# Kernel optimization log

Measured on AMD Instinct MI355X. Metric: run time of the kernel, lower is better.

## Reference

```python
import jax, jax.numpy as jnp
import numpy as np

V, E, H, F, A, L = 32000, 256, 512, 512, 256, 49  # vocab, embed, hidden, feature, attn, n_locations
B, T = 64, 32


def setup_inputs() -> dict:
    key = jax.random.key(0)
    ks = jax.random.split(key, 16)
    s = lambda k, sh: (jax.random.normal(k, sh, jnp.float32) * 0.02)
    embedding = s(ks[0], (V, E)).at[0].set(0.0)  # padding_idx=0 row zeroed
    return dict(
        image_feats=jax.random.normal(ks[1], (B, L, F), jnp.float32),
        caption_in=jax.random.randint(ks[2], (B, T), 0, V, dtype=jnp.int32),
        embedding=embedding,
        W_init_h=s(ks[3], (F, H)), b_init_h=jnp.zeros((H,), jnp.float32),
        W_init_c=s(ks[4], (F, H)), b_init_c=jnp.zeros((H,), jnp.float32),
        W_feat=s(ks[5], (F, A)), b_feat=jnp.zeros((A,), jnp.float32),
        W_hid=s(ks[6], (H, A)), b_hid=jnp.zeros((A,), jnp.float32),
        W_score=s(ks[7], (A,)), b_score=jnp.zeros((), jnp.float32),
        W_ih=s(ks[8], (E + F, 4 * H)), b_ih=jnp.zeros((4 * H,), jnp.float32),
        W_hh=s(ks[9], (H, 4 * H)), b_hh=jnp.zeros((4 * H,), jnp.float32),
        W_out=s(ks[10], (H, V)), b_out=jnp.zeros((V,), jnp.float32),
    )


def reference(image_feats, caption_in, embedding,
              W_init_h, b_init_h, W_init_c, b_init_c,
              W_feat, b_feat, W_hid, b_hid, W_score, b_score,
              W_ih, b_ih, W_hh, b_hh, W_out, b_out):
    # init_hidden_state: mean over spatial locations -> two linears
    mean_feats = image_feats.mean(axis=1)                      # (B, F)
    h0 = mean_feats @ W_init_h + b_init_h                      # (B, H)
    c0 = mean_feats @ W_init_c + b_init_c                      # (B, H)
    embs = embedding[caption_in]                               # (B, T, E); dropout = identity (eval)
    feat_proj = image_feats @ W_feat + b_feat                  # (B, L, A) - invariant over t, precompute

    def step(carry, emb_t):
        h, c = carry
        # additive attention
        energy = jnp.tanh(feat_proj + (h @ W_hid + b_hid)[:, None, :])   # (B, L, A)
        scores = energy @ W_score + b_score                              # (B, L)
        alpha = jax.nn.softmax(scores, axis=1)                           # (B, L)
        context = jnp.einsum('bl,blf->bf', alpha, image_feats)           # (B, F)
        # LSTMCell (torch gate order i, f, g, o)
        x = jnp.concatenate([emb_t, context], axis=1)                    # (B, E+F)
        gates = x @ W_ih + b_ih + h @ W_hh + b_hh                        # (B, 4H)
        i, f, g, o = jnp.split(gates, 4, axis=1)
        i = jax.nn.sigmoid(i); f = jax.nn.sigmoid(f); o = jax.nn.sigmoid(o)
        c_new = f * c + i * jnp.tanh(g)
        h_new = o * jnp.tanh(c_new)
        logits_t = h_new @ W_out + b_out                                 # (B, V); dropout = identity
        return (h_new, c_new), (logits_t, alpha)

    _, (logits, alphas) = jax.lax.scan(step, (h0, c0), jnp.swapaxes(embs, 0, 1))
    predictions = jnp.swapaxes(logits, 0, 1)   # (B, T, V)
    all_alphas = jnp.swapaxes(alphas, 0, 1)    # (B, T, L)
    return predictions, all_alphas
```

## Files before the change

### kernel.cpp

```cpp
#include <hip/hip_runtime.h>
#include <hip/hip_bf16.h>

typedef _Float16 f16;
typedef _Float16 f16x8 __attribute__((ext_vector_type(8)));
typedef _Float16 f16x4 __attribute__((ext_vector_type(4)));
typedef _Float16 f16x2 __attribute__((ext_vector_type(2)));
typedef float f32x4 __attribute__((ext_vector_type(4)));
typedef unsigned long long ull;

#define B_ 64
#define T_ 32
#define L_ 49
#define F_ 512
#define H_ 512
#define A_ 256
#define E_ 256
#define V_ 32000
#define G4 2048
#define NG 64
#define NLOG 125
#define SLOT 16

#define ALOAD32(p)     __hip_atomic_load((const unsigned*)(p), __ATOMIC_RELAXED, __HIP_MEMORY_SCOPE_AGENT)
#define ASTORE32(p, v) __hip_atomic_store((unsigned*)(p), (v), __ATOMIC_RELAXED, __HIP_MEMORY_SCOPE_AGENT)
#define ASTORE64(p, v) __hip_atomic_store((ull*)(p), (v), __ATOMIC_RELAXED, __HIP_MEMORY_SCOPE_AGENT)

#if defined(__has_builtin)
#if __has_builtin(__builtin_amdgcn_fdot2)
#define HAS_FDOT2 1
#endif
#endif

#define NB_EMBG 256
#define NB_Q    128
#define NB_INIT 64
#define NB_FP   196

struct Smem128 { f16 As[128][40]; f16 Bs[128][40]; };

__global__ __launch_bounds__(256) void k_prep(
    const float* __restrict__ image_feats, const int* __restrict__ caption,
    const float* __restrict__ embedding,
    const float* __restrict__ W_init_h, const float* __restrict__ b_init_h,
    const float* __restrict__ W_init_c, const float* __restrict__ b_init_c,
    const float* __restrict__ W_feat, const float* __restrict__ b_feat,
    const float* __restrict__ W_hid, const float* __restrict__ W_ih,
    const float* __restrict__ b_ih, const float* __restrict__ b_hh,
    f16* __restrict__ embP, f16* __restrict__ Whidp,
    f16* __restrict__ hslab, float* __restrict__ c_cur,
    float* __restrict__ featproj) {
    __shared__ __align__(16) char smem[32768];
    int bid = blockIdx.x, tid = threadIdx.x;
    int r = bid;
    if (r < NB_EMBG) {
        Smem128* sm = (Smem128*)smem;
        int mtiles = B_ * T_ / 128;
        int m0 = (r % mtiles) * 128, n0 = (r / mtiles) * 128;
        int lane = tid & 63, wave = tid >> 6;
        int wr = (wave >> 1) * 64, wc = (wave & 1) * 64;
        int frow = lane & 15, fk = (lane >> 4) * 8;
        int ra = tid >> 2, ka = (tid & 3) * 8;
        int kb = tid >> 3, nb = (tid & 7) * 16;
        int tok0 = caption[m0 + ra], tok1 = caption[m0 + 64 + ra];
        f32x4 acc[4][4];
#pragma unroll
        for (int i = 0; i < 4; ++i)
#pragma unroll
            for (int j = 0; j < 4; ++j) { acc[i][j][0]=0.f; acc[i][j][1]=0.f; acc[i][j][2]=0.f; acc[i][j][3]=0.f; }
        for (int k0 = 0; k0 < E_; k0 += 32) {
            float4 e00 = *(const float4*)&embedding[(size_t)tok0 * E_ + k0 + ka];
            float4 e01 = *(const float4*)&embedding[(size_t)tok0 * E_ + k0 + ka + 4];
            float4 e10 = *(const float4*)&embedding[(size_t)tok1 * E_ + k0 + ka];
            float4 e11 = *(const float4*)&embedding[(size_t)tok1 * E_ + k0 + ka + 4];
            const float* wrow = W_ih + (size_t)(k0 + kb) * G4 + n0 + nb;
            float4 w0 = *(const float4*)wrow;
            float4 w1 = *(const float4*)(wrow + 4);
            float4 w2 = *(const float4*)(wrow + 8);
            float4 w3 = *(const float4*)(wrow + 12);
            __syncthreads();
            {
                f16x8 a0 = {(f16)e00.x,(f16)e00.y,(f16)e00.z,(f16)e00.w,
                            (f16)e01.x,(f16)e01.y,(f16)e01.z,(f16)e01.w};
                f16x8 a1 = {(f16)e10.x,(f16)e10.y,(f16)e10.z,(f16)e10.w,
                            (f16)e11.x,(f16)e11.y,(f16)e11.z,(f16)e11.w};
                *(f16x8*)&sm->As[ra][ka] = a0;
                *(f16x8*)&sm->As[64 + ra][ka] = a1;
                float wv[16] = {w0.x,w0.y,w0.z,w0.w, w1.x,w1.y,w1.z,w1.w,
                                w2.x,w2.y,w2.z,w2.w, w3.x,w3.y,w3.z,w3.w};
#pragma unroll
                for (int j = 0; j < 16; ++j) sm->Bs[nb + j][kb] = (f16)wv[j];
            }
            __syncthreads();
            f16x8 av[4], bv[4];
#pragma unroll
            for (int i = 0; i < 4; ++i) {
                av[i] = *(f16x8*)&sm->As[wr + i * 16 + frow][fk];
                bv[i] = *(f16x8*)&sm->Bs[wc + i * 16 + frow][fk];
            }
#pragma unroll
            for (int mi = 0; mi < 4; ++mi)
#pragma unroll
                for (int ni = 0; ni < 4; ++ni)
                    acc[mi][ni] = __builtin_amdgcn_mfma_f32_16x16x32_f16(av[mi], bv[ni], acc[mi][ni], 0, 0, 0);
        }
        int rq = (lane >> 4) * 4;
#pragma unroll
        for (int mi = 0; mi < 4; ++mi)
#pragma unroll
            for (int ni = 0; ni < 4; ++ni) {
                int cc = n0 + wc + ni * 16 + frow;
                float badd = b_ih[cc] + b_hh[cc];
#pragma unroll
                for (int rr2 = 0; rr2 < 4; ++rr2) {
                    int rr = m0 + wr + mi * 16 + rq + rr2;
                    embP[((size_t)rr * 512 + (cc & 511)) * 4 + (cc >> 9)] =
                        (f16)(acc[mi][ni][rr2] + badd);
                }
            }
        return;
    }
    r -= NB_EMBG;
    if (r < NB_Q) {
        int k4 = r;
        f16 buf[4];
#pragma unroll
        for (int j = 0; j < 4; ++j) buf[j] = (f16)W_hid[(size_t)(4 * k4 + j) * 256 + tid];
        *(f16x4*)&Whidp[((size_t)k4 * 256 + tid) * 4] = *(f16x4*)buf;
        return;
    }
    r -= NB_Q;
    if (r < NB_INIT) {
        float* mean = (float*)smem;
        int b = r;
        for (int f = tid; f < F_; f += 256) {
            float s = 0.f;
            for (int l = 0; l < L_; ++l) s += image_feats[((size_t)b * L_ + l) * F_ + f];
            mean[f] = s * (1.f / 49.f);
        }
        __syncthreads();
        for (int h = tid; h < H_; h += 256) {
            float a = b_init_h[h], c = b_init_c[h];
            for (int k = 0; k < F_; ++k) {
                float m = mean[k];
                a += m * W_init_h[k * H_ + h];
                c += m * W_init_c[k * H_ + h];
            }
            hslab[(size_t)b * H_ + h] = (f16)a;
            c_cur[b * H_ + h] = c;
        }
        return;
    }
    r -= NB_INIT;
    {
        float (*fs)[F_] = (float(*)[F_])smem;
        int r0 = r * 16;
        for (int i = tid; i < 16 * F_; i += 256)
            fs[i >> 9][i & 511] = image_feats[(size_t)r0 * F_ + i];
        __syncthreads();
        float acc[16];
#pragma unroll
        for (int q = 0; q < 16; ++q) acc[q] = 0.f;
        for (int k = 0; k < F_; ++k) {
            float w = W_feat[k * A_ + tid];
#pragma unroll
            for (int q = 0; q < 16; ++q) acc[q] += fs[q][k] * w;
        }
        float bb = b_feat[tid];
#pragma unroll
        for (int q = 0; q < 16; ++q) featproj[(size_t)(r0 + q) * A_ + tid] = acc[q] + bb;
    }
}

struct GateSm {
    float fp[L_][A_];
    unsigned fe[L_ * 256];
    float ea[A_];
    float ws[A_];
    float sc[64];
    float alpha[64];
    unsigned hL[256];
};
struct GemmSm {
    f16 w[32][512];
    f16 w2[32][512];
    union {
        f16 hs[64][512];
        f16 hwT16[64][40];
    } u;
};
struct LogSm { f16 hs[128][512]; };

__device__ __forceinline__ void wait_n(const unsigned* flags, int n, unsigned target) {
    int tid = threadIdx.x;
    if (tid < n) {
        const unsigned* p = flags + tid * SLOT;
        while (ALOAD32(p) < target) __builtin_amdgcn_s_sleep(1);
    }
    asm volatile("" ::: "memory");
    __syncthreads();
}
__device__ __forceinline__ void wait_n_slow(const unsigned* flags, int n, unsigned target) {
    int tid = threadIdx.x;
    if (tid < n) {
        const unsigned* p = flags + tid * SLOT;
        while (ALOAD32(p) < target) __builtin_amdgcn_s_sleep(8);
    }
    asm volatile("" ::: "memory");
    __syncthreads();
}

__device__ __forceinline__ float sigm(float x) { return 1.f / (1.f + __expf(-x)); }
__device__ __forceinline__ float tanh_f(float x) { return 1.f - 2.f / (1.f + __expf(2.f * x)); }

__global__ __launch_bounds__(256, 1) void k_steps(
    const float* __restrict__ W_hh, const float* __restrict__ W_ih,
    const f16* __restrict__ Whidp,
    const float* __restrict__ featproj, const float* __restrict__ image_feats,
    const float* __restrict__ b_hid,
    const float* __restrict__ W_score, const float* __restrict__ b_score,
    const f16* __restrict__ embP, const float* __restrict__ c_cur,
    f16* __restrict__ hslab, f16* __restrict__ ctxslab, f16* __restrict__ hwcslab,
    const float* __restrict__ W_out, f16* __restrict__ WoutT,
    const float* __restrict__ b_out,
    float* __restrict__ preds, float* __restrict__ out_alpha,
    unsigned* __restrict__ gateflag, unsigned* __restrict__ ctxflag,
    unsigned* __restrict__ gemmflag) {
    __shared__ __align__(16) char smraw[sizeof(LogSm)];
    int bid = blockIdx.x, tid = threadIdx.x;

    if (bid < 64) {
        int b = bid;
        GateSm* S = (GateSm*)smraw;
        for (int i = tid; i < L_ * A_; i += 256)
            ((float*)S->fp)[i] = featproj[(size_t)b * L_ * A_ + i];
        {
            const float2* src = (const float2*)(image_feats + (size_t)b * L_ * F_);
            for (int i = tid; i < L_ * 256; i += 256) {
                float2 v = src[i];
                union { f16 h[2]; unsigned u; } pk;
                pk.h[0] = (f16)v.x; pk.h[1] = (f16)v.y;
                S->fe[i] = pk.u;
            }
        }
        S->ws[tid] = W_score[tid];
        float bhid_r = b_hid[tid];
        float bsc = b_score[0];
        S->hL[tid] = ((const unsigned*)hslab)[(size_t)b * 256 + tid];
        float cs0 = c_cur[b * H_ + 2 * tid], cs1 = c_cur[b * H_ + 2 * tid + 1];
        const f16x4* wp4 = (const f16x4*)Whidp;
        int wv = tid >> 6, ln = tid & 63;
        __syncthreads();

        for (int t = 0; t < T_; ++t) {
            {
                float acc = bhid_r;
#pragma unroll 16
                for (int k4 = 0; k4 < 128; ++k4) {
                    union { f16x4 v; f16x2 p[2]; } w;
                    w.v = wp4[(size_t)k4 * 256 + tid];
                    union { unsigned u; f16x2 v; } h0, h1;
                    h0.u = S->hL[2 * k4];
                    h1.u = S->hL[2 * k4 + 1];
#ifdef HAS_FDOT2
                    acc = __builtin_amdgcn_fdot2(w.p[0], h0.v, acc, false);
                    acc = __builtin_amdgcn_fdot2(w.p[1], h1.v, acc, false);
#else
                    acc += (float)w.p[0].x * (float)h0.v.x + (float)w.p[0].y * (float)h0.v.y;
                    acc += (float)w.p[1].x * (float)h1.v.x + (float)w.p[1].y * (float)h1.v.y;
#endif
                }
                S->ea[tid] = acc;
            }
            __syncthreads();
            for (int l = wv; l < L_; l += 4) {
                float p = 0.f;
#pragma unroll
                for (int q = 0; q < 4; ++q) {
                    int j = ln + q * 64;
                    p += tanh_f(S->fp[l][j] + S->ea[j]) * S->ws[j];
                }
#pragma unroll
                for (int off = 32; off > 0; off >>= 1) p += __shfl_xor(p, off);
                if (ln == 0) S->sc[l] = p;
            }
            __syncthreads();
            if (tid < 64) {
                float v = (tid < L_) ? S->sc[tid] + bsc : -3.4e38f;
                float m = v;
#pragma unroll
                for (int off = 32; off > 0; off >>= 1) m = fmaxf(m, __shfl_xor(m, off));
                float e = (tid < L_) ? __expf(v - m) : 0.f;
                float s = e;
#pragma unroll
                for (int off = 32; off > 0; off >>= 1) s += __shfl_xor(s, off);
                if (tid < L_) {
                    float al = e / s;
                    S->alpha[tid] = al;
                    out_alpha[((size_t)b * T_ + t) * L_ + tid] = al;
                }
            }
            __syncthreads();
            {
                float c0 = 0.f, c1 = 0.f;
#pragma unroll 7
                for (int l = 0; l < L_; ++l) {
                    float a = S->alpha[l];
                    union { unsigned u; f16x2 v; } fv;
                    fv.u = S->fe[l * 256 + tid];
                    c0 += a * (float)fv.v.x;
                    c1 += a * (float)fv.v.y;
                }
                union { f16 h[2]; unsigned u; } pk;
                pk.h[0] = (f16)c0; pk.h[1] = (f16)c1;
                ASTORE32((unsigned*)ctxslab + ((size_t)t * B_ + b) * 256 + tid, pk.u);
            }
            __syncthreads();
            if (tid == 0) ASTORE32(&ctxflag[b * SLOT], (unsigned)(t + 1));
            f16x8 ep = *(const f16x8*)&embP[((size_t)b * T_ + t) * G4 + 8 * tid];
            wait_n(gemmflag, NG, (unsigned)(t + 1));
            {
                f16x8 hw = *(const f16x8*)&hwcslab[((size_t)t * B_ + b) * G4 + 8 * tid];
                float gA[8];
#pragma unroll
                for (int i = 0; i < 8; ++i) gA[i] = (float)hw[i] + (float)ep[i];
                float cn0 = sigm(gA[1]) * cs0 + sigm(gA[0]) * tanh_f(gA[2]);
                float cn1 = sigm(gA[5]) * cs1 + sigm(gA[4]) * tanh_f(gA[6]);
                float hn0 = sigm(gA[3]) * tanh_f(cn0);
                float hn1 = sigm(gA[7]) * tanh_f(cn1);
                cs0 = cn0; cs1 = cn1;
                union { f16 h[2]; unsigned u; } pk;
                pk.h[0] = (f16)hn0; pk.h[1] = (f16)hn1;
                S->hL[tid] = pk.u;
                ASTORE32((unsigned*)hslab + ((size_t)(t + 1) * B_ + b) * 256 + tid, pk.u);
            }
            __syncthreads();
            if (tid == 0)
                ASTORE32(&gateflag[b * SLOT], (unsigned)(t + 2));
        }
    } else if (bid < 64 + NG) {
        int g = bid - 64;
        GemmSm* S = (GemmSm*)smraw;
        for (int rowbase = 0; rowbase < 512; rowbase += 256) {
            int k = rowbase + tid;
            const float* wh = W_hh + (size_t)k * G4 + 8 * g;
            const float* wi = W_ih + (size_t)(E_ + k) * G4 + 8 * g;
            int ch = k >> 3, j = k & 7;
#pragma unroll
            for (int q = 0; q < 4; ++q) {
                float4 v0 = *(const float4*)(wh + q * 512);
                float4 v1 = *(const float4*)(wh + q * 512 + 4);
                float4 u0 = *(const float4*)(wi + q * 512);
                float4 u1 = *(const float4*)(wi + q * 512 + 4);
                float vv[8] = {v0.x,v0.y,v0.z,v0.w, v1.x,v1.y,v1.z,v1.w};
                float uu[8] = {u0.x,u0.y,u0.z,u0.w, u1.x,u1.y,u1.z,u1.w};
#pragma unroll
                for (int d = 0; d < 8; ++d) {
                    int r = d * 4 + q;
                    S->w[r][((ch ^ (r & 7)) << 3) + j]  = (f16)vv[d];
                    S->w2[r][((ch ^ (r & 7)) << 3) + j] = (f16)uu[d];
                }
            }
        }
        int wvv = tid >> 6, lane = tid & 63;
        int frow = lane & 15, q = lane >> 4, sw = frow & 7, rq = q * 4;
        int mb = (wvv >> 1) * 32, c16 = (wvv & 1) * 16;
        int bo = tid >> 2, cq = (tid & 3) * 8;
        __syncthreads();

        for (int t = 0; t < T_; ++t) {
            if (t) wait_n(gateflag, 64, (unsigned)(t + 1));
            {
                const f16* hsrc = hslab + (size_t)t * B_ * H_;
#pragma unroll
                for (int i = 0; i < 16; ++i) {
                    int idx = i * 256 + tid;
                    int r = idx >> 6, ch = idx & 63;
                    *(f16x8*)&S->u.hs[r][(ch ^ (r & 7)) * 8] =
                        *(const f16x8*)&hsrc[(size_t)r * H_ + ch * 8];
                }
            }
            __syncthreads();
            f32x4 a4[2];
            a4[0][0]=0.f; a4[0][1]=0.f; a4[0][2]=0.f; a4[0][3]=0.f;
            a4[1][0]=0.f; a4[1][1]=0.f; a4[1][2]=0.f; a4[1][3]=0.f;
#pragma unroll
            for (int kk = 0; kk < 16; ++kk) {
                int ch = ((kk * 4 + q) ^ sw) * 8;
                f16x8 bv = *(f16x8*)&S->w[c16 + frow][ch];
                f16x8 av0 = *(f16x8*)&S->u.hs[mb + frow][ch];
                f16x8 av1 = *(f16x8*)&S->u.hs[mb + 16 + frow][ch];
                a4[0] = __builtin_amdgcn_mfma_f32_16x16x32_f16(av0, bv, a4[0], 0, 0, 0);
                a4[1] = __builtin_amdgcn_mfma_f32_16x16x32_f16(av1, bv, a4[1], 0, 0, 0);
            }
            wait_n(ctxflag, 64, (unsigned)(t + 1));
            {
                const f16* csrc = ctxslab + (size_t)t * B_ * F_;
#pragma unroll
                for (int i = 0; i < 16; ++i) {
                    int idx = i * 256 + tid;
                    int r = idx >> 6, ch = idx & 63;
                    *(f16x8*)&S->u.hs[r][(ch ^ (r & 7)) * 8] =
                        *(const f16x8*)&csrc[(size_t)r * F_ + ch * 8];
                }
            }
            __syncthreads();
#pragma unroll
            for (int kk = 0; kk < 16; ++kk) {
                int ch = ((kk * 4 + q) ^ sw) * 8;
                f16x8 bv = *(f16x8*)&S->w2[c16 + frow][ch];
                f16x8 av0 = *(f16x8*)&S->u.hs[mb + frow][ch];
                f16x8 av1 = *(f16x8*)&S->u.hs[mb + 16 + frow][ch];
                a4[0] = __builtin_amdgcn_mfma_f32_16x16x32_f16(av0, bv, a4[0], 0, 0, 0);
                a4[1] = __builtin_amdgcn_mfma_f32_16x16x32_f16(av1, bv, a4[1], 0, 0, 0);
            }
            __syncthreads();
#pragma unroll
            for (int mi = 0; mi < 2; ++mi)
#pragma unroll
                for (int r = 0; r < 4; ++r)
                    S->u.hwT16[mb + mi * 16 + rq + r][c16 + frow] = (f16)a4[mi][r];
            __syncthreads();
            {
                f16* dst = hwcslab + ((size_t)t * B_ + bo) * G4 + 32 * g + cq;
                union { f16 h[4]; ull u; } pk0, pk1;
                *(f16x4*)pk0.h = *(f16x4*)&S->u.hwT16[bo][cq];
                *(f16x4*)pk1.h = *(f16x4*)&S->u.hwT16[bo][cq + 4];
                ASTORE64(dst, pk0.u);
                ASTORE64(dst + 4, pk1.u);
            }
            __syncthreads();
            if (tid == 0)
                ASTORE32(&gemmflag[g * SLOT], (unsigned)(t + 1));
        }
    } else {
        int nt = bid - 64 - NG;
        int n0 = nt * 256;
        LogSm* S = (LogSm*)smraw;
        int wvv = tid >> 6, lane = tid & 63;
        int frow = lane & 15, q = lane >> 4, sw = frow & 7, rq = q * 4;

        {
            float (*ls)[33] = (float(*)[33])smraw;
            int rr = tid >> 3, cs = (tid & 7) * 4;
            int cr = tid >> 3, rs = (tid & 7) * 4;
            for (int c0 = 0; c0 < 256; c0 += 32)
                for (int k0 = 0; k0 < 512; k0 += 32) {
                    float4 v = *(const float4*)&W_out[(size_t)(k0 + rr) * V_ + n0 + c0 + cs];
                    __syncthreads();
                    ls[rr][cs] = v.x; ls[rr][cs + 1] = v.y; ls[rr][cs + 2] = v.z; ls[rr][cs + 3] = v.w;
                    __syncthreads();
                    f16x4 o = {(f16)ls[rs][cr], (f16)ls[rs + 1][cr],
                               (f16)ls[rs + 2][cr], (f16)ls[rs + 3][cr]};
                    *(f16x4*)&WoutT[(size_t)(n0 + c0 + cr) * 512 + k0 + rs] = o;
                }
            __syncthreads();
        }

        for (int tc = 0; tc < T_ / 2; ++tc) {
            wait_n_slow(gateflag, 64, (unsigned)(2 * tc + 3));
            {
                const f16* hsrc = hslab + (size_t)(2 * tc + 1) * B_ * H_;
#pragma unroll
                for (int i = 0; i < 32; ++i) {
                    int idx = i * 256 + tid;
                    int r = idx >> 6, ch = idx & 63;
                    *(f16x8*)&S->hs[r][(ch ^ (r & 7)) * 8] =
                        *(const f16x8*)&hsrc[(size_t)r * H_ + ch * 8];
                }
            }
            __syncthreads();
            f32x4 acc[8][4];
#pragma unroll
            for (int mi = 0; mi < 8; ++mi)
#pragma unroll
                for (int ni = 0; ni < 4; ++ni) { acc[mi][ni][0]=0.f; acc[mi][ni][1]=0.f; acc[mi][ni][2]=0.f; acc[mi][ni][3]=0.f; }
#pragma unroll 2
            for (int kk = 0; kk < 16; ++kk) {
                int ch = ((kk * 4 + q) ^ sw) * 8;
                f16x8 av[8], bv[4];
#pragma unroll
                for (int mi = 0; mi < 8; ++mi)
                    av[mi] = *(f16x8*)&S->hs[mi * 16 + frow][ch];
#pragma unroll
                for (int ni = 0; ni < 4; ++ni)
                    bv[ni] = *(const f16x8*)&WoutT[(size_t)(n0 + wvv * 64 + ni * 16 + frow) * 512 + kk * 32 + q * 8];
#pragma unroll
                for (int mi = 0; mi < 8; ++mi)
#pragma unroll
                    for (int ni = 0; ni < 4; ++ni)
                        acc[mi][ni] = __builtin_amdgcn_mfma_f32_16x16x32_f16(av[mi], bv[ni], acc[mi][ni], 0, 0, 0);
            }
#pragma unroll
            for (int ni = 0; ni < 4; ++ni) {
                int cc = n0 + wvv * 64 + ni * 16 + frow;
                float badd = b_out[cc];
#pragma unroll
                for (int mi = 0; mi < 8; ++mi)
#pragma unroll
                    for (int r = 0; r < 4; ++r) {
                        int rr = mi * 16 + rq + r;
                        int tt = 2 * tc + (rr >> 6), bb2 = rr & 63;
                        preds[((size_t)bb2 * T_ + tt) * V_ + cc] = acc[mi][ni][r] + badd;
                    }
            }
            __syncthreads();
        }
    }
}

extern "C" void kernel_launch(void* const* d_in, const int* in_sizes, int n_in,
                              void* d_out, int out_size, void* d_ws, size_t ws_size,
                              hipStream_t stream) {
    const float* image_feats = (const float*)d_in[0];
    const int*   caption     = (const int*)d_in[1];
    const float* embedding   = (const float*)d_in[2];
    const float* W_init_h    = (const float*)d_in[3];
    const float* b_init_h    = (const float*)d_in[4];
    const float* W_init_c    = (const float*)d_in[5];
    const float* b_init_c    = (const float*)d_in[6];
    const float* W_feat      = (const float*)d_in[7];
    const float* b_feat      = (const float*)d_in[8];
    const float* W_hid       = (const float*)d_in[9];
    const float* b_hid       = (const float*)d_in[10];
    const float* W_score     = (const float*)d_in[11];
    const float* b_score     = (const float*)d_in[12];
    const float* W_ih        = (const float*)d_in[13];
    const float* b_ih        = (const float*)d_in[14];
    const float* W_hh        = (const float*)d_in[15];
    const float* b_hh        = (const float*)d_in[16];
    const float* W_out       = (const float*)d_in[17];
    const float* b_out       = (const float*)d_in[18];

    float* preds = (float*)d_out;
    float* out_alpha = preds + (size_t)B_ * T_ * V_;

    size_t off = 0;
    char* base = (char*)d_ws;
    auto carve = [&](size_t bytes) {
        void* p = base + off;
        off += (bytes + 255) & ~(size_t)255;
        return p;
    };
    f16* embP       = (f16*)carve((size_t)B_ * T_ * G4 * 2);
    float* featproj = (float*)carve((size_t)B_ * L_ * A_ * 4);
    float* c_cur    = (float*)carve((size_t)B_ * H_ * 4);
    f16* hslab      = (f16*)carve((size_t)(T_ + 1) * B_ * H_ * 2);
    f16* ctxslab    = (f16*)carve((size_t)T_ * B_ * F_ * 2);
    f16* hwcslab    = (f16*)carve((size_t)T_ * B_ * G4 * 2);
    unsigned* flags = (unsigned*)carve((64 + 64 + NG) * SLOT * 4);
    f16* WoutT      = (f16*)carve((size_t)V_ * H_ * 2);
    f16* Whidp      = (f16*)carve((size_t)H_ * A_ * 2);
    unsigned* gateflag = flags;
    unsigned* ctxflag  = flags + 64 * SLOT;
    unsigned* gemmflag = flags + 128 * SLOT;
    (void)ws_size; (void)in_sizes; (void)n_in; (void)out_size;

    hipMemsetAsync(flags, 0, (64 + 64 + NG) * SLOT * 4, stream);
    hipLaunchKernelGGL(k_prep, dim3(NB_EMBG + NB_Q + NB_INIT + NB_FP), dim3(256), 0, stream,
                       image_feats, caption, embedding,
                       W_init_h, b_init_h, W_init_c, b_init_c,
                       W_feat, b_feat, W_hid, W_ih, b_ih, b_hh,
                       embP, Whidp, hslab, c_cur, featproj);
    hipLaunchKernelGGL(k_steps, dim3(64 + NG + NLOG), dim3(256), 0, stream,
                       W_hh, W_ih, Whidp, featproj, image_feats, b_hid,
                       W_score, b_score, embP, c_cur,
                       hslab, ctxslab, hwcslab,
                       W_out, WoutT, b_out, preds, out_alpha,
                       gateflag, ctxflag, gemmflag);
}
```

Before: 624.3 us.

## Move init, feat-proj and W_hid packing into persistent kernel; split recurrent GEMM

```diff
diff --git a/kernel.cpp b/kernel.cpp
--- a/kernel.cpp
+++ b/kernel.cpp
@@ -31,149 +31,84 @@
 #endif
 #endif
 
-#define NB_EMBG 256
-#define NB_Q    128
-#define NB_INIT 64
-#define NB_FP   196
-
 struct Smem128 { f16 As[128][40]; f16 Bs[128][40]; };
 
 __global__ __launch_bounds__(256) void k_prep(
-    const float* __restrict__ image_feats, const int* __restrict__ caption,
-    const float* __restrict__ embedding,
-    const float* __restrict__ W_init_h, const float* __restrict__ b_init_h,
-    const float* __restrict__ W_init_c, const float* __restrict__ b_init_c,
-    const float* __restrict__ W_feat, const float* __restrict__ b_feat,
-    const float* __restrict__ W_hid, const float* __restrict__ W_ih,
+    const int* __restrict__ caption, const float* __restrict__ embedding,
+    const float* __restrict__ W_ih,
     const float* __restrict__ b_ih, const float* __restrict__ b_hh,
-    f16* __restrict__ embP, f16* __restrict__ Whidp,
-    f16* __restrict__ hslab, float* __restrict__ c_cur,
-    float* __restrict__ featproj) {
-    __shared__ __align__(16) char smem[32768];
-    int bid = blockIdx.x, tid = threadIdx.x;
-    int r = bid;
-    if (r < NB_EMBG) {
-        Smem128* sm = (Smem128*)smem;
-        int mtiles = B_ * T_ / 128;
-        int m0 = (r % mtiles) * 128, n0 = (r / mtiles) * 128;
-        int lane = tid & 63, wave = tid >> 6;
-        int wr = (wave >> 1) * 64, wc = (wave & 1) * 64;
-        int frow = lane & 15, fk = (lane >> 4) * 8;
-        int ra = tid >> 2, ka = (tid & 3) * 8;
-        int kb = tid >> 3, nb = (tid & 7) * 16;
-        int tok0 = caption[m0 + ra], tok1 = caption[m0 + 64 + ra];
-        f32x4 acc[4][4];
-#pragma unroll
-        for (int i = 0; i < 4; ++i)
-#pragma unroll
-            for (int j = 0; j < 4; ++j) { acc[i][j][0]=0.f; acc[i][j][1]=0.f; acc[i][j][2]=0.f; acc[i][j][3]=0.f; }
-        for (int k0 = 0; k0 < E_; k0 += 32) {
-            float4 e00 = *(const float4*)&embedding[(size_t)tok0 * E_ + k0 + ka];
-            float4 e01 = *(const float4*)&embedding[(size_t)tok0 * E_ + k0 + ka + 4];
-            float4 e10 = *(const float4*)&embedding[(size_t)tok1 * E_ + k0 + ka];
-            float4 e11 = *(const float4*)&embedding[(size_t)tok1 * E_ + k0 + ka + 4];
-            const float* wrow = W_ih + (size_t)(k0 + kb) * G4 + n0 + nb;
-            float4 w0 = *(const float4*)wrow;
-            float4 w1 = *(const float4*)(wrow + 4);
-            float4 w2 = *(const float4*)(wrow + 8);
-            float4 w3 = *(const float4*)(wrow + 12);
-            __syncthreads();
-            {
-                f16x8 a0 = {(f16)e00.x,(f16)e00.y,(f16)e00.z,(f16)e00.w,
-                            (f16)e01.x,(f16)e01.y,(f16)e01.z,(f16)e01.w};
-                f16x8 a1 = {(f16)e10.x,(f16)e10.y,(f16)e10.z,(f16)e10.w,
-                            (f16)e11.x,(f16)e11.y,(f16)e11.z,(f16)e11.w};
-                *(f16x8*)&sm->As[ra][ka] = a0;
-                *(f16x8*)&sm->As[64 + ra][ka] = a1;
-                float wv[16] = {w0.x,w0.y,w0.z,w0.w, w1.x,w1.y,w1.z,w1.w,
-                                w2.x,w2.y,w2.z,w2.w, w3.x,w3.y,w3.z,w3.w};
-#pragma unroll
-                for (int j = 0; j < 16; ++j) sm->Bs[nb + j][kb] = (f16)wv[j];
-            }
-            __syncthreads();
-            f16x8 av[4], bv[4];
-#pragma unroll
-            for (int i = 0; i < 4; ++i) {
-                av[i] = *(f16x8*)&sm->As[wr + i * 16 + frow][fk];
-                bv[i] = *(f16x8*)&sm->Bs[wc + i * 16 + frow][fk];
-            }
-#pragma unroll
-            for (int mi = 0; mi < 4; ++mi)
-#pragma unroll
-                for (int ni = 0; ni < 4; ++ni)
-                    acc[mi][ni] = __builtin_amdgcn_mfma_f32_16x16x32_f16(av[mi], bv[ni], acc[mi][ni], 0, 0, 0);
-        }
-        int rq = (lane >> 4) * 4;
+    f16* __restrict__ embP) {
+    __shared__ Smem128 sm;
+    int tid = threadIdx.x;
+    int mtiles = B_ * T_ / 128;
+    int m0 = ((int)blockIdx.x % mtiles) * 128, n0 = ((int)blockIdx.x / mtiles) * 128;
+    int lane = tid & 63, wave = tid >> 6;
+    int wr = (wave >> 1) * 64, wc = (wave & 1) * 64;
+    int frow = lane & 15, fk = (lane >> 4) * 8;
+    int ra = tid >> 2, ka = (tid & 3) * 8;
+    int kb = tid >> 3, nb = (tid & 7) * 16;
+    int tok0 = caption[m0 + ra], tok1 = caption[m0 + 64 + ra];
+    f32x4 acc[4][4];
+#pragma unroll
+    for (int i = 0; i < 4; ++i)
+#pragma unroll
+        for (int j = 0; j < 4; ++j) { acc[i][j][0]=0.f; acc[i][j][1]=0.f; acc[i][j][2]=0.f; acc[i][j][3]=0.f; }
+    for (int k0 = 0; k0 < E_; k0 += 32) {
+        float4 e00 = *(const float4*)&embedding[(size_t)tok0 * E_ + k0 + ka];
+        float4 e01 = *(const float4*)&embedding[(size_t)tok0 * E_ + k0 + ka + 4];
+        float4 e10 = *(const float4*)&embedding[(size_t)tok1 * E_ + k0 + ka];
+        float4 e11 = *(const float4*)&embedding[(size_t)tok1 * E_ + k0 + ka + 4];
+        const float* wrow = W_ih + (size_t)(k0 + kb) * G4 + n0 + nb;
+        float4 w0 = *(const float4*)wrow;
+        float4 w1 = *(const float4*)(wrow + 4);
+        float4 w2 = *(const float4*)(wrow + 8);
+        float4 w3 = *(const float4*)(wrow + 12);
+        __syncthreads();
+        {
+            f16x8 a0 = {(f16)e00.x,(f16)e00.y,(f16)e00.z,(f16)e00.w,
+                        (f16)e01.x,(f16)e01.y,(f16)e01.z,(f16)e01.w};
+            f16x8 a1 = {(f16)e10.x,(f16)e10.y,(f16)e10.z,(f16)e10.w,
+                        (f16)e11.x,(f16)e11.y,(f16)e11.z,(f16)e11.w};
+            *(f16x8*)&sm.As[ra][ka] = a0;
+            *(f16x8*)&sm.As[64 + ra][ka] = a1;
+            float wv[16] = {w0.x,w0.y,w0.z,w0.w, w1.x,w1.y,w1.z,w1.w,
+                            w2.x,w2.y,w2.z,w2.w, w3.x,w3.y,w3.z,w3.w};
+#pragma unroll
+            for (int j = 0; j < 16; ++j) sm.Bs[nb + j][kb] = (f16)wv[j];
+        }
+        __syncthreads();
+        f16x8 av[4], bv[4];
+#pragma unroll
+        for (int i = 0; i < 4; ++i) {
+            av[i] = *(f16x8*)&sm.As[wr + i * 16 + frow][fk];
+            bv[i] = *(f16x8*)&sm.Bs[wc + i * 16 + frow][fk];
+        }
 #pragma unroll
         for (int mi = 0; mi < 4; ++mi)
 #pragma unroll
-            for (int ni = 0; ni < 4; ++ni) {
-                int cc = n0 + wc + ni * 16 + frow;
-                float badd = b_ih[cc] + b_hh[cc];
-#pragma unroll
-                for (int rr2 = 0; rr2 < 4; ++rr2) {
-                    int rr = m0 + wr + mi * 16 + rq + rr2;
-                    embP[((size_t)rr * 512 + (cc & 511)) * 4 + (cc >> 9)] =
-                        (f16)(acc[mi][ni][rr2] + badd);
-                }
-            }
-        return;
+            for (int ni = 0; ni < 4; ++ni)
+                acc[mi][ni] = __builtin_amdgcn_mfma_f32_16x16x32_f16(av[mi], bv[ni], acc[mi][ni], 0, 0, 0);
     }
-    r -= NB_EMBG;
-    if (r < NB_Q) {
-        int k4 = r;
-        f16 buf[4];
-#pragma unroll
-        for (int j = 0; j < 4; ++j) buf[j] = (f16)W_hid[(size_t)(4 * k4 + j) * 256 + tid];
-        *(f16x4*)&Whidp[((size_t)k4 * 256 + tid) * 4] = *(f16x4*)buf;
-        return;
-    }
-    r -= NB_Q;
-    if (r < NB_INIT) {
-        float* mean = (float*)smem;
-        int b = r;
-        for (int f = tid; f < F_; f += 256) {
-            float s = 0.f;
-            for (int l = 0; l < L_; ++l) s += image_feats[((size_t)b * L_ + l) * F_ + f];
-            mean[f] = s * (1.f / 49.f);
-        }
-        __syncthreads();
-        for (int h = tid; h < H_; h += 256) {
-            float a = b_init_h[h], c = b_init_c[h];
-            for (int k = 0; k < F_; ++k) {
-                float m = mean[k];
-                a += m * W_init_h[k * H_ + h];
-                c += m * W_init_c[k * H_ + h];
-            }
-            hslab[(size_t)b * H_ + h] = (f16)a;
-            c_cur[b * H_ + h] = c;
-        }
-        return;
-    }
-    r -= NB_INIT;
-    {
-        float (*fs)[F_] = (float(*)[F_])smem;
-        int r0 = r * 16;
-        for (int i = tid; i < 16 * F_; i += 256)
-            fs[i >> 9][i & 511] = image_feats[(size_t)r0 * F_ + i];
-        __syncthreads();
-        float acc[16];
-#pragma unroll
-        for (int q = 0; q < 16; ++q) acc[q] = 0.f;
-        for (int k = 0; k < F_; ++k) {
-            float w = W_feat[k * A_ + tid];
-#pragma unroll
-            for (int q = 0; q < 16; ++q) acc[q] += fs[q][k] * w;
-        }
-        float bb = b_feat[tid];
-#pragma unroll
-        for (int q = 0; q < 16; ++q) featproj[(size_t)(r0 + q) * A_ + tid] = acc[q] + bb;
-    }
+    int rq = (lane >> 4) * 4;
+#pragma unroll
+    for (int mi = 0; mi < 4; ++mi)
+#pragma unroll
+        for (int ni = 0; ni < 4; ++ni) {
+            int cc = n0 + wc + ni * 16 + frow;
+            float badd = b_ih[cc] + b_hh[cc];
+#pragma unroll
+            for (int rr2 = 0; rr2 < 4; ++rr2) {
+                int rr = m0 + wr + mi * 16 + rq + rr2;
+                embP[((size_t)rr * 512 + (cc & 511)) * 4 + (cc >> 9)] =
+                    (f16)(acc[mi][ni][rr2] + badd);
+            }
+        }
 }
 
 struct GateSm {
     float fp[L_][A_];
     unsigned fe[L_ * 256];
+    float mean[F_];
     float ea[A_];
     float ws[A_];
     float sc[64];
@@ -214,25 +149,28 @@
 
 __global__ __launch_bounds__(256, 1) void k_steps(
     const float* __restrict__ W_hh, const float* __restrict__ W_ih,
-    const f16* __restrict__ Whidp,
-    const float* __restrict__ featproj, const float* __restrict__ image_feats,
+    const float* __restrict__ W_hid, f16* __restrict__ Whidp,
+    const float* __restrict__ image_feats,
+    const float* __restrict__ W_feat, const float* __restrict__ b_feat,
+    const float* __restrict__ W_init_h, const float* __restrict__ b_init_h,
+    const float* __restrict__ W_init_c, const float* __restrict__ b_init_c,
     const float* __restrict__ b_hid,
     const float* __restrict__ W_score, const float* __restrict__ b_score,
-    const f16* __restrict__ embP, const float* __restrict__ c_cur,
-    f16* __restrict__ hslab, f16* __restrict__ ctxslab, f16* __restrict__ hwcslab,
+    const f16* __restrict__ embP,
+    f16* __restrict__ hslab, f16* __restrict__ ctxslab,
+    f16* __restrict__ hwslab, f16* __restrict__ cwslab,
     const float* __restrict__ W_out, f16* __restrict__ WoutT,
     const float* __restrict__ b_out,
     float* __restrict__ preds, float* __restrict__ out_alpha,
     unsigned* __restrict__ gateflag, unsigned* __restrict__ ctxflag,
-    unsigned* __restrict__ gemmflag) {
+    unsigned* __restrict__ hwflag, unsigned* __restrict__ cwflag,
+    unsigned* __restrict__ whidflag) {
     __shared__ __align__(16) char smraw[sizeof(LogSm)];
     int bid = blockIdx.x, tid = threadIdx.x;
 
     if (bid < 64) {
         int b = bid;
         GateSm* S = (GateSm*)smraw;
-        for (int i = tid; i < L_ * A_; i += 256)
-            ((float*)S->fp)[i] = featproj[(size_t)b * L_ * A_ + i];
         {
             const float2* src = (const float2*)(image_feats + (size_t)b * L_ * F_);
             for (int i = tid; i < L_ * 256; i += 256) {
@@ -245,11 +183,60 @@
         S->ws[tid] = W_score[tid];
         float bhid_r = b_hid[tid];
         float bsc = b_score[0];
-        S->hL[tid] = ((const unsigned*)hslab)[(size_t)b * 256 + tid];
-        float cs0 = c_cur[b * H_ + 2 * tid], cs1 = c_cur[b * H_ + 2 * tid + 1];
+        __syncthreads();
+        {
+            float bf = b_feat[tid];
+            for (int lt = 0; lt < 7; ++lt) {
+                float acc[7] = {0.f,0.f,0.f,0.f,0.f,0.f,0.f};
+                for (int k2 = 0; k2 < 256; ++k2) {
+                    float w0 = W_feat[(size_t)(2 * k2) * A_ + tid];
+                    float w1 = W_feat[(size_t)(2 * k2 + 1) * A_ + tid];
+#pragma unroll
+                    for (int j = 0; j < 7; ++j) {
+                        union { unsigned u; f16x2 v; } fv;
+                        fv.u = S->fe[(lt * 7 + j) * 256 + k2];
+                        acc[j] += w0 * (float)fv.v.x + w1 * (float)fv.v.y;
+                    }
+                }
+#pragma unroll
+                for (int j = 0; j < 7; ++j) S->fp[lt * 7 + j][tid] = acc[j] + bf;
+            }
+        }
+        {
+            float m0 = 0.f, m1 = 0.f;
+#pragma unroll 7
+            for (int l = 0; l < L_; ++l) {
+                union { unsigned u; f16x2 v; } fv;
+                fv.u = S->fe[l * 256 + tid];
+                m0 += (float)fv.v.x; m1 += (float)fv.v.y;
+            }
+            S->mean[2 * tid]     = m0 * (1.f / 49.f);
+            S->mean[2 * tid + 1] = m1 * (1.f / 49.f);
+        }
+        __syncthreads();
+        int j0 = 2 * tid;
+        float cs0, cs1;
+        {
+            float h0a = b_init_h[j0], h0b = b_init_h[j0 + 1];
+            float c0a = b_init_c[j0], c0b = b_init_c[j0 + 1];
+            for (int k = 0; k < F_; ++k) {
+                float m = S->mean[k];
+                float2 wh = *(const float2*)&W_init_h[(size_t)k * H_ + j0];
+                float2 wc = *(const float2*)&W_init_c[(size_t)k * H_ + j0];
+                h0a += m * wh.x; h0b += m * wh.y;
+                c0a += m * wc.x; c0b += m * wc.y;
+            }
+            cs0 = c0a; cs1 = c0b;
+            union { f16 h[2]; unsigned u; } pk;
+            pk.h[0] = (f16)h0a; pk.h[1] = (f16)h0b;
+            S->hL[tid] = pk.u;
+            ASTORE32((unsigned*)hslab + (size_t)b * 256 + tid, pk.u);
+        }
+        __syncthreads();
+        if (tid == 0) ASTORE32(&gateflag[b * SLOT], 1u);
+        wait_n(whidflag, NG, 1u);
         const f16x4* wp4 = (const f16x4*)Whidp;
         int wv = tid >> 6, ln = tid & 63;
-        __syncthreads();
 
         for (int t = 0; t < T_; ++t) {
             {
@@ -317,12 +304,19 @@
             __syncthreads();
             if (tid == 0) ASTORE32(&ctxflag[b * SLOT], (unsigned)(t + 1));
             f16x8 ep = *(const f16x8*)&embP[((size_t)b * T_ + t) * G4 + 8 * tid];
-            wait_n(gemmflag, NG, (unsigned)(t + 1));
-            {
-                f16x8 hw = *(const f16x8*)&hwcslab[((size_t)t * B_ + b) * G4 + 8 * tid];
+            wait_n(hwflag, NG, (unsigned)(t + 1));
+            float gp[8];
+            {
+                f16x8 hw = *(const f16x8*)&hwslab[((size_t)t * B_ + b) * G4 + 8 * tid];
+#pragma unroll
+                for (int i = 0; i < 8; ++i) gp[i] = (float)hw[i] + (float)ep[i];
+            }
+            wait_n(cwflag, NG, (unsigned)(t + 1));
+            {
+                f16x8 cw = *(const f16x8*)&cwslab[((size_t)t * B_ + b) * G4 + 8 * tid];
                 float gA[8];
 #pragma unroll
-                for (int i = 0; i < 8; ++i) gA[i] = (float)hw[i] + (float)ep[i];
+                for (int i = 0; i < 8; ++i) gA[i] = gp[i] + (float)cw[i];
                 float cn0 = sigm(gA[1]) * cs0 + sigm(gA[0]) * tanh_f(gA[2]);
                 float cn1 = sigm(gA[5]) * cs1 + sigm(gA[4]) * tanh_f(gA[6]);
                 float hn0 = sigm(gA[3]) * tanh_f(cn0);
@@ -340,6 +334,21 @@
     } else if (bid < 64 + NG) {
         int g = bid - 64;
         GemmSm* S = (GemmSm*)smraw;
+        {
+#pragma unroll
+            for (int s = 0; s < 2; ++s) {
+                int k4 = 2 * g + s;
+                f16 buf[4];
+#pragma unroll
+                for (int j = 0; j < 4; ++j)
+                    buf[j] = (f16)W_hid[(size_t)(4 * k4 + j) * A_ + tid];
+                union { f16 h[4]; ull u; } pk;
+                *(f16x4*)pk.h = *(f16x4*)buf;
+                ASTORE64((ull*)&Whidp[((size_t)k4 * 256 + tid) * 4], pk.u);
+            }
+        }
+        __syncthreads();
+        if (tid == 0) ASTORE32(&whidflag[g * SLOT], 1u);
         for (int rowbase = 0; rowbase < 512; rowbase += 256) {
             int k = rowbase + tid;
             const float* wh = W_hh + (size_t)k * G4 + 8 * g;
@@ -368,7 +377,7 @@
         __syncthreads();
 
         for (int t = 0; t < T_; ++t) {
-            if (t) wait_n(gateflag, 64, (unsigned)(t + 1));
+            wait_n(gateflag, 64, (unsigned)(t + 1));
             {
                 const f16* hsrc = hslab + (size_t)t * B_ * H_;
 #pragma unroll
@@ -392,6 +401,23 @@
                 a4[0] = __builtin_amdgcn_mfma_f32_16x16x32_f16(av0, bv, a4[0], 0, 0, 0);
                 a4[1] = __builtin_amdgcn_mfma_f32_16x16x32_f16(av1, bv, a4[1], 0, 0, 0);
             }
+            __syncthreads();
+#pragma unroll
+            for (int mi = 0; mi < 2; ++mi)
+#pragma unroll
+                for (int r = 0; r < 4; ++r)
+                    S->u.hwT16[mb + mi * 16 + rq + r][c16 + frow] = (f16)a4[mi][r];
+            __syncthreads();
+            {
+                f16* dst = hwslab + ((size_t)t * B_ + bo) * G4 + 32 * g + cq;
+                union { f16 h[4]; ull u; } pk0, pk1;
+                *(f16x4*)pk0.h = *(f16x4*)&S->u.hwT16[bo][cq];
+                *(f16x4*)pk1.h = *(f16x4*)&S->u.hwT16[bo][cq + 4];
+                ASTORE64(dst, pk0.u);
+                ASTORE64(dst + 4, pk1.u);
+            }
+            __syncthreads();
+            if (tid == 0) ASTORE32(&hwflag[g * SLOT], (unsigned)(t + 1));
             wait_n(ctxflag, 64, (unsigned)(t + 1));
             {
                 const f16* csrc = ctxslab + (size_t)t * B_ * F_;
@@ -404,24 +430,27 @@
                 }
             }
             __syncthreads();
+            f32x4 c4[2];
+            c4[0][0]=0.f; c4[0][1]=0.f; c4[0][2]=0.f; c4[0][3]=0.f;
+            c4[1][0]=0.f; c4[1][1]=0.f; c4[1][2]=0.f; c4[1][3]=0.f;
 #pragma unroll
             for (int kk = 0; kk < 16; ++kk) {
                 int ch = ((kk * 4 + q) ^ sw) * 8;
                 f16x8 bv = *(f16x8*)&S->w2[c16 + frow][ch];
                 f16x8 av0 = *(f16x8*)&S->u.hs[mb + frow][ch];
                 f16x8 av1 = *(f16x8*)&S->u.hs[mb + 16 + frow][ch];
-                a4[0] = __builtin_amdgcn_mfma_f32_16x16x32_f16(av0, bv, a4[0], 0, 0, 0);
-                a4[1] = __builtin_amdgcn_mfma_f32_16x16x32_f16(av1, bv, a4[1], 0, 0, 0);
+                c4[0] = __builtin_amdgcn_mfma_f32_16x16x32_f16(av0, bv, c4[0], 0, 0, 0);
+                c4[1] = __builtin_amdgcn_mfma_f32_16x16x32_f16(av1, bv, c4[1], 0, 0, 0);
             }
             __syncthreads();
 #pragma unroll
             for (int mi = 0; mi < 2; ++mi)
 #pragma unroll
                 for (int r = 0; r < 4; ++r)
-                    S->u.hwT16[mb + mi * 16 + rq + r][c16 + frow] = (f16)a4[mi][r];
-            __syncthreads();
-            {
-                f16* dst = hwcslab + ((size_t)t * B_ + bo) * G4 + 32 * g + cq;
+                    S->u.hwT16[mb + mi * 16 + rq + r][c16 + frow] = (f16)c4[mi][r];
+            __syncthreads();
+            {
+                f16* dst = cwslab + ((size_t)t * B_ + bo) * G4 + 32 * g + cq;
                 union { f16 h[4]; ull u; } pk0, pk1;
                 *(f16x4*)pk0.h = *(f16x4*)&S->u.hwT16[bo][cq];
                 *(f16x4*)pk1.h = *(f16x4*)&S->u.hwT16[bo][cq + 4];
@@ -429,8 +458,7 @@
                 ASTORE64(dst + 4, pk1.u);
             }
             __syncthreads();
-            if (tid == 0)
-                ASTORE32(&gemmflag[g * SLOT], (unsigned)(t + 1));
+            if (tid == 0) ASTORE32(&cwflag[g * SLOT], (unsigned)(t + 1));
         }
     } else {
         int nt = bid - 64 - NG;
@@ -542,29 +570,28 @@
         return p;
     };
     f16* embP       = (f16*)carve((size_t)B_ * T_ * G4 * 2);
-    float* featproj = (float*)carve((size_t)B_ * L_ * A_ * 4);
-    float* c_cur    = (float*)carve((size_t)B_ * H_ * 4);
     f16* hslab      = (f16*)carve((size_t)(T_ + 1) * B_ * H_ * 2);
     f16* ctxslab    = (f16*)carve((size_t)T_ * B_ * F_ * 2);
-    f16* hwcslab    = (f16*)carve((size_t)T_ * B_ * G4 * 2);
-    unsigned* flags = (unsigned*)carve((64 + 64 + NG) * SLOT * 4);
+    f16* hwslab     = (f16*)carve((size_t)T_ * B_ * G4 * 2);
+    f16* cwslab     = (f16*)carve((size_t)T_ * B_ * G4 * 2);
+    unsigned* flags = (unsigned*)carve(5 * 64 * SLOT * 4);
     f16* WoutT      = (f16*)carve((size_t)V_ * H_ * 2);
     f16* Whidp      = (f16*)carve((size_t)H_ * A_ * 2);
     unsigned* gateflag = flags;
     unsigned* ctxflag  = flags + 64 * SLOT;
-    unsigned* gemmflag = flags + 128 * SLOT;
+    unsigned* hwflag   = flags + 128 * SLOT;
+    unsigned* cwflag   = flags + 192 * SLOT;
+    unsigned* whidflag = flags + 256 * SLOT;
     (void)ws_size; (void)in_sizes; (void)n_in; (void)out_size;
 
-    hipMemsetAsync(flags, 0, (64 + 64 + NG) * SLOT * 4, stream);
-    hipLaunchKernelGGL(k_prep, dim3(NB_EMBG + NB_Q + NB_INIT + NB_FP), dim3(256), 0, stream,
-                       image_feats, caption, embedding,
-                       W_init_h, b_init_h, W_init_c, b_init_c,
-                       W_feat, b_feat, W_hid, W_ih, b_ih, b_hh,
-                       embP, Whidp, hslab, c_cur, featproj);
+    hipMemsetAsync(flags, 0, 5 * 64 * SLOT * 4, stream);
+    hipLaunchKernelGGL(k_prep, dim3((B_ * T_ / 128) * (G4 / 128)), dim3(256), 0, stream,
+                       caption, embedding, W_ih, b_ih, b_hh, embP);
     hipLaunchKernelGGL(k_steps, dim3(64 + NG + NLOG), dim3(256), 0, stream,
-                       W_hh, W_ih, Whidp, featproj, image_feats, b_hid,
-                       W_score, b_score, embP, c_cur,
-                       hslab, ctxslab, hwcslab,
+                       W_hh, W_ih, W_hid, Whidp, image_feats,
+                       W_feat, b_feat, W_init_h, b_init_h, W_init_c, b_init_c,
+                       b_hid, W_score, b_score, embP,
+                       hslab, ctxslab, hwslab, cwslab,
                        W_out, WoutT, b_out, preds, out_alpha,
-                       gateflag, ctxflag, gemmflag);
+                       gateflag, ctxflag, hwflag, cwflag, whidflag);
 }
```

Result: slower. 816.1 us (+30.7%).
